# Performance work log

Measured on AMD Instinct MI355X. Metric: run time of the kernel, lower is better.

Reference implementation:

```python
import jax, jax.numpy as jnp
import numpy as np

B, K = 32768, 9  # batch, sudoku size


def setup_inputs() -> dict:
    key = jax.random.key(0)
    k1, = jax.random.split(key, 1)
    # binary possibility masks, as the module expects 0/1 sudoku tensors
    sudoku = (jax.random.uniform(k1, (B, K, K, K)) > 0.5).astype(jnp.float32)
    return {
        "sudoku": sudoku,
        "recursion_mask": jnp.zeros((B, K, K, K), jnp.float32),
        "recursion_index": jnp.ones((B, 1, 1, 1), jnp.float32),
        "conv_w": jnp.ones((1, K, 1, 1), jnp.float32),
        "conv_b": jnp.zeros((1,), jnp.float32),
    }


def reference(sudoku, recursion_mask, recursion_index, conv_w, conv_b):
    b = sudoku.shape[0]

    def conv1x1(x):  # channel-sum 1x1 conv: [b,K,K,K] -> [b,1,K,K]
        return jnp.sum(x * conv_w.reshape(1, K, 1, 1), axis=1, keepdims=True) + conv_b.reshape(1, 1, 1, 1)

    # number of candidates in each cell, minus 1, negated; empty cells pushed to -K
    nic = jax.nn.relu(conv1x1(sudoku) - 1.0)
    mask0 = jnp.clip(1.0 - jnp.abs(nic), 0.0, 1.0) * (-K)  # NNCompare(nic, 0) * -K
    nic = mask0 - nic  # [b,1,K,K]

    # MaxPool2d(K) + MaxUnpool2d(K): one-hot at the (first) argmax cell of the board
    idx = jnp.argmax(nic.reshape(b, K * K), axis=-1)
    current_cell_mask = jax.nn.one_hot(idx, K * K, dtype=sudoku.dtype).reshape(b, 1, K, K)

    # SudokuSelectOneVariant: per-cell MaxPool1d(K)+unpool over the number channel
    s = jnp.transpose(sudoku, (0, 3, 2, 1)).reshape(b, K * K, K)  # [b, cells, numbers]
    mval = jnp.max(s, axis=-1)
    midx = jnp.argmax(s, axis=-1)
    filt = jax.nn.one_hot(midx, K, dtype=sudoku.dtype) * mval[..., None]
    filt = jnp.transpose(filt.reshape(b, K, K, K), (0, 3, 2, 1))  # back to [b,K,K,K]
    one_variant = filt * current_cell_mask

    # mark all other candidates in the chosen cell, remove them from sudoku
    cell_mask = jnp.clip(conv1x1(one_variant), 0.0, 1.0)
    one_recursion_mask = sudoku * cell_mask * (1.0 - one_variant)  # NNAnd(.., NNNot(..))
    recursion_mask = jnp.maximum(recursion_mask, recursion_index * one_recursion_mask)
    recursion_mask = jnp.maximum(recursion_mask, (recursion_index - 1.0) * one_variant)
    sudoku_out = sudoku * (1.0 - one_recursion_mask)
    return sudoku_out, recursion_mask, recursion_index + 1.0
```

## Files before the change

kernel.cpp:

```cpp
#include <hip/hip_runtime.h>

typedef float v4f __attribute__((ext_vector_type(4)));

#define BDIM   256
#define KK     9
#define CELLS  81
#define BOARD  729
#define BPB    4
#define CHUNK  (BPB * BOARD)
#define LDSW   736

__global__ __launch_bounds__(BDIM) void sudoku_iter_kernel(
    const float* __restrict__ sudoku,
    const float* __restrict__ rmask,
    const float* __restrict__ rindex,
    const float* __restrict__ conv_w,
    const float* __restrict__ conv_b,
    float* __restrict__ out,
    int Btot)
{
    __shared__ float lds_s[BPB * LDSW];

    const int tid  = threadIdx.x;
    const int wave = tid >> 6;
    const int lane = tid & 63;
    const int blk  = blockIdx.x;
    const size_t base = (size_t)blk * CHUNK;

    const int fstart = wave * BOARD;
    const int g_lo   = (fstart + 3) >> 2;
    const int g_hi   = (fstart + BOARD) >> 2;
    const int h      = 4 * g_lo - fstart;
    const int t      = fstart + BOARD - 4 * g_hi;
    const int n4     = g_hi - g_lo;

    const v4f* gs4 = (const v4f*)(sudoku + base);
    const v4f* gr4 = (const v4f*)(rmask  + base);
    v4f s4[3], r4[3];
    bool act[3];
    #pragma unroll
    for (int i = 0; i < 3; ++i) {
        int k2 = lane + 64 * i;
        act[i] = (k2 < n4);
        if (act[i]) s4[i] = gs4[g_lo + k2];
    }
    const bool hasH = (lane < h);
    const bool hasT = (lane >= 8) && (lane < 8 + t);
    const int  eH   = lane;
    const int  eT   = BOARD - t + (lane - 8);
    float sh = 0.f, st = 0.f, rh = 0.f, rt = 0.f;
    if (hasH) sh = sudoku[base + fstart + eH];
    if (hasT) st = sudoku[base + fstart + eT];
    #pragma unroll
    for (int i = 0; i < 3; ++i) {
        if (act[i]) r4[i] = gr4[g_lo + lane + 64 * i];
    }
    if (hasH) rh = rmask[base + fstart + eH];
    if (hasT) rt = rmask[base + fstart + eT];
    float ri0 = (lane == 0) ? rindex[blk * BPB + wave] : 0.f;

    float wreg[KK];
    #pragma unroll
    for (int n = 0; n < KK; ++n) wreg[n] = conv_w[n];
    const float bias = conv_b[0];
    const float cmp  = fminf(fmaxf(bias, 0.f), 1.f);

    float* bs  = lds_s + wave * LDSW + (4 - h);
    v4f*   bs4 = (v4f*)(lds_s + wave * LDSW + 4);
    #pragma unroll
    for (int i = 0; i < 3; ++i) {
        if (act[i]) bs4[lane + 64 * i] = s4[i];
    }
    if (hasH) bs[eH] = sh;
    if (hasT) bs[eT] = st;

    float v0; int i0;
    {
        const int cell = lane;
        float cnt = bias;
        #pragma unroll
        for (int n = 0; n < KK; ++n) cnt += bs[n * CELLS + cell] * wreg[n];
        float nic = fmaxf(cnt - 1.f, 0.f);
        float m0  = fminf(fmaxf(1.f - nic, 0.f), 1.f) * (-(float)KK);
        v0 = m0 - nic; i0 = cell;
    }
    if (lane < CELLS - 64) {
        const int cell = lane + 64;
        float cnt = bias;
        #pragma unroll
        for (int n = 0; n < KK; ++n) cnt += bs[n * CELLS + cell] * wreg[n];
        float nic = fmaxf(cnt - 1.f, 0.f);
        float m0  = fminf(fmaxf(1.f - nic, 0.f), 1.f) * (-(float)KK);
        float v1 = m0 - nic;
        if (v1 > v0) { v0 = v1; i0 = cell; }
    }
    #pragma unroll
    for (int off = 32; off > 0; off >>= 1) {
        float ov = __shfl_xor(v0, off, 64);
        int   oi = __shfl_xor(i0, off, 64);
        if (ov > v0 || (ov == v0 && oi < i0)) { v0 = ov; i0 = oi; }
    }
    float m = 0.f, cms = 0.f; int es = 0, cellstar = 0;
    if (lane == 0) {
        cellstar = i0;
        m = bs[cellstar]; int nstar = 0;
        #pragma unroll
        for (int n = 1; n < KK; ++n) {
            float v = bs[n * CELLS + cellstar];
            if (v > m) { m = v; nstar = n; }
        }
        es  = nstar * CELLS + cellstar;
        cms = fminf(fmaxf(m * wreg[nstar] + bias, 0.f), 1.f);
    }
    m        = __shfl(m, 0, 64);
    cms      = __shfl(cms, 0, 64);
    es       = __shfl(es, 0, 64);
    cellstar = __shfl(cellstar, 0, 64);
    const float ri = __shfl(ri0, 0, 64);

    v4f* os4 = (v4f*)(out + base);
    v4f* or4 = (v4f*)(out + (size_t)Btot * BOARD + base);
    const int ebase = h + 4 * lane;
    const int cbase = ebase % CELLS;
    const int iadd[3] = {0, 13, 26};

    #pragma unroll
    for (int i = 0; i < 3; ++i) {
        if (act[i]) {
            float so[4], ro[4];
            const float* sp = (const float*)&s4[i];
            const float* rp = (const float*)&r4[i];
            #pragma unroll
            for (int j = 0; j < 4; ++j) {
                int e = ebase + 256 * i + j;
                int cell = cbase + iadd[i] + j;
                if (cell >= CELLS) cell -= CELLS;
                float s  = sp[j];
                float rm = rp[j];
                float ov  = (e == es) ? m : 0.f;
                float cm  = (cell == cellstar) ? cms : cmp;
                float orm = s * cm * (1.f - ov);
                float rmo = fmaxf(rm, ri * orm);
                rmo = fmaxf(rmo, (ri - 1.f) * ov);
                so[j] = s * (1.f - orm);
                ro[j] = rmo;
            }
            v4f sv; sv.x = so[0]; sv.y = so[1]; sv.z = so[2]; sv.w = so[3];
            v4f rv; rv.x = ro[0]; rv.y = ro[1]; rv.z = ro[2]; rv.w = ro[3];
            __builtin_nontemporal_store(sv, &os4[g_lo + lane + 64 * i]);
            __builtin_nontemporal_store(rv, &or4[g_lo + lane + 64 * i]);
        }
    }
    if (hasH | hasT) {
        int   e  = hasH ? eH : eT;
        float s  = hasH ? sh : st;
        float rm = hasH ? rh : rt;
        int cell = (e >= 648) ? (e - 648) : e;
        float ov  = (e == es) ? m : 0.f;
        float cm  = (cell == cellstar) ? cms : cmp;
        float orm = s * cm * (1.f - ov);
        float rmo = fmaxf(rm, ri * orm);
        rmo = fmaxf(rmo, (ri - 1.f) * ov);
        __builtin_nontemporal_store(s * (1.f - orm), out + base + fstart + e);
        __builtin_nontemporal_store(rmo, out + (size_t)Btot * BOARD + base + fstart + e);
    }

    if (lane == 0) {
        out[(size_t)Btot * BOARD * 2 + (size_t)blk * BPB + wave] = ri + 1.f;
    }
}

extern "C" void kernel_launch(void* const* d_in, const int* in_sizes, int n_in,
                              void* d_out, int out_size, void* d_ws, size_t ws_size,
                              hipStream_t stream) {
    const float* sudoku = (const float*)d_in[0];
    const float* rmask  = (const float*)d_in[1];
    const float* rindex = (const float*)d_in[2];
    const float* conv_w = (const float*)d_in[3];
    const float* conv_b = (const float*)d_in[4];
    float* out = (float*)d_out;

    const int Btot = in_sizes[2];
    const int nblocks = Btot / BPB;

    sudoku_iter_kernel<<<nblocks, BDIM, 0, stream>>>(
        sudoku, rmask, rindex, conv_w, conv_b, out, Btot);
}
```

Before: 336.4 us.

## Drop LDS staging; read cell columns directly from global and reload after argmax

Removes the shared-memory board buffer. Each wave now loads its 9 channel values per cell straight from global memory (strided scalar loads), computes the argmax, then each lane reads the chosen cell column itself instead of lane 0 broadcasting it. The vectorised sudoku/rmask loads now happen after the argmax and re-read the board, which is meant to hit in cache. This trades LDS traffic and shuffles for extra global (cache) loads and a serialised second read phase.

Result: no change. 330.1 us (-1.9%).

```diff
diff --git a/kernel.cpp b/kernel.cpp
--- a/kernel.cpp
+++ b/kernel.cpp
@@ -7,8 +7,6 @@
 #define CELLS  81
 #define BOARD  729
 #define BPB    4
-#define CHUNK  (BPB * BOARD)
-#define LDSW   736
 
 __global__ __launch_bounds__(BDIM) void sudoku_iter_kernel(
     const float* __restrict__ sudoku,
@@ -19,80 +17,44 @@
     float* __restrict__ out,
     int Btot)
 {
-    __shared__ float lds_s[BPB * LDSW];
+    const int tid   = threadIdx.x;
+    const int lane  = tid & 63;
+    const int board = blockIdx.x * BPB + (tid >> 6);
+    const unsigned fs = (unsigned)board * BOARD;
+    const float* bs = sudoku + fs;
 
-    const int tid  = threadIdx.x;
-    const int wave = tid >> 6;
-    const int lane = tid & 63;
-    const int blk  = blockIdx.x;
-    const size_t base = (size_t)blk * CHUNK;
-
-    const int fstart = wave * BOARD;
-    const int g_lo   = (fstart + 3) >> 2;
-    const int g_hi   = (fstart + BOARD) >> 2;
-    const int h      = 4 * g_lo - fstart;
-    const int t      = fstart + BOARD - 4 * g_hi;
-    const int n4     = g_hi - g_lo;
-
-    const v4f* gs4 = (const v4f*)(sudoku + base);
-    const v4f* gr4 = (const v4f*)(rmask  + base);
-    v4f s4[3], r4[3];
-    bool act[3];
+    float a[KK];
     #pragma unroll
-    for (int i = 0; i < 3; ++i) {
-        int k2 = lane + 64 * i;
-        act[i] = (k2 < n4);
-        if (act[i]) s4[i] = gs4[g_lo + k2];
-    }
-    const bool hasH = (lane < h);
-    const bool hasT = (lane >= 8) && (lane < 8 + t);
-    const int  eH   = lane;
-    const int  eT   = BOARD - t + (lane - 8);
-    float sh = 0.f, st = 0.f, rh = 0.f, rt = 0.f;
-    if (hasH) sh = sudoku[base + fstart + eH];
-    if (hasT) st = sudoku[base + fstart + eT];
+    for (int n = 0; n < KK; ++n) a[n] = bs[n * CELLS + lane];
+    const bool hi = (lane < CELLS - 64);
+    float b[KK];
     #pragma unroll
-    for (int i = 0; i < 3; ++i) {
-        if (act[i]) r4[i] = gr4[g_lo + lane + 64 * i];
-    }
-    if (hasH) rh = rmask[base + fstart + eH];
-    if (hasT) rt = rmask[base + fstart + eT];
-    float ri0 = (lane == 0) ? rindex[blk * BPB + wave] : 0.f;
+    for (int n = 0; n < KK; ++n) b[n] = hi ? bs[n * CELLS + 64 + lane] : 0.f;
 
     float wreg[KK];
     #pragma unroll
     for (int n = 0; n < KK; ++n) wreg[n] = conv_w[n];
     const float bias = conv_b[0];
     const float cmp  = fminf(fmaxf(bias, 0.f), 1.f);
-
-    float* bs  = lds_s + wave * LDSW + (4 - h);
-    v4f*   bs4 = (v4f*)(lds_s + wave * LDSW + 4);
-    #pragma unroll
-    for (int i = 0; i < 3; ++i) {
-        if (act[i]) bs4[lane + 64 * i] = s4[i];
-    }
-    if (hasH) bs[eH] = sh;
-    if (hasT) bs[eT] = st;
+    const float ri   = rindex[board];
 
     float v0; int i0;
     {
-        const int cell = lane;
         float cnt = bias;
         #pragma unroll
-        for (int n = 0; n < KK; ++n) cnt += bs[n * CELLS + cell] * wreg[n];
+        for (int n = 0; n < KK; ++n) cnt += a[n] * wreg[n];
         float nic = fmaxf(cnt - 1.f, 0.f);
         float m0  = fminf(fmaxf(1.f - nic, 0.f), 1.f) * (-(float)KK);
-        v0 = m0 - nic; i0 = cell;
+        v0 = m0 - nic; i0 = lane;
     }
-    if (lane < CELLS - 64) {
-        const int cell = lane + 64;
+    if (hi) {
         float cnt = bias;
         #pragma unroll
-        for (int n = 0; n < KK; ++n) cnt += bs[n * CELLS + cell] * wreg[n];
+        for (int n = 0; n < KK; ++n) cnt += b[n] * wreg[n];
         float nic = fmaxf(cnt - 1.f, 0.f);
         float m0  = fminf(fmaxf(1.f - nic, 0.f), 1.f) * (-(float)KK);
         float v1 = m0 - nic;
-        if (v1 > v0) { v0 = v1; i0 = cell; }
+        if (v1 > v0) { v0 = v1; i0 = lane + 64; }
     }
     #pragma unroll
     for (int off = 32; off > 0; off >>= 1) {
@@ -100,28 +62,49 @@
         int   oi = __shfl_xor(i0, off, 64);
         if (ov > v0 || (ov == v0 && oi < i0)) { v0 = ov; i0 = oi; }
     }
-    float m = 0.f, cms = 0.f; int es = 0, cellstar = 0;
-    if (lane == 0) {
-        cellstar = i0;
-        m = bs[cellstar]; int nstar = 0;
-        #pragma unroll
-        for (int n = 1; n < KK; ++n) {
-            float v = bs[n * CELLS + cellstar];
-            if (v > m) { m = v; nstar = n; }
-        }
-        es  = nstar * CELLS + cellstar;
-        cms = fminf(fmaxf(m * wreg[nstar] + bias, 0.f), 1.f);
+    const int cellstar = __builtin_amdgcn_readfirstlane(i0);
+
+    float m = bs[cellstar]; int nstar = 0;
+    #pragma unroll
+    for (int n = 1; n < KK; ++n) {
+        float v = bs[n * CELLS + cellstar];
+        if (v > m) { m = v; nstar = n; }
     }
-    m        = __shfl(m, 0, 64);
-    cms      = __shfl(cms, 0, 64);
-    es       = __shfl(es, 0, 64);
-    cellstar = __shfl(cellstar, 0, 64);
-    const float ri = __shfl(ri0, 0, 64);
+    const int   es  = nstar * CELLS + cellstar;
+    const float cms = fminf(fmaxf(m * wreg[nstar] + bias, 0.f), 1.f);
 
-    v4f* os4 = (v4f*)(out + base);
-    v4f* or4 = (v4f*)(out + (size_t)Btot * BOARD + base);
-    const int ebase = h + 4 * lane;
-    const int cbase = ebase % CELLS;
+    const unsigned G_lo = (fs + 3) >> 2;
+    const unsigned G_hi = (fs + BOARD) >> 2;
+    const int h  = (int)(4 * G_lo - fs);
+    const int t  = (int)(fs + BOARD - 4 * G_hi);
+    const int n4 = (int)(G_hi - G_lo);
+
+    const v4f* gs4 = (const v4f*)sudoku;
+    const v4f* gr4 = (const v4f*)rmask;
+    v4f* os4 = (v4f*)out;
+    v4f* or4 = (v4f*)(out + (size_t)Btot * BOARD);
+
+    v4f s4[3], r4[3];
+    bool act[3];
+    #pragma unroll
+    for (int i = 0; i < 3; ++i) {
+        int k = lane + 64 * i;
+        act[i] = (k < n4);
+        if (act[i]) s4[i] = gs4[G_lo + k];
+    }
+    #pragma unroll
+    for (int i = 0; i < 3; ++i) {
+        if (act[i]) r4[i] = gr4[G_lo + lane + 64 * i];
+    }
+    const bool hasH = (lane < h);
+    const bool hasT = (lane >= 8) && (lane < 8 + t);
+    const int  eH   = lane;
+    const int  eT   = BOARD - t + (lane - 8);
+    float shd = 0.f, std_ = 0.f, rhd = 0.f, rtd = 0.f;
+    if (hasH) { shd = sudoku[fs + eH]; rhd = rmask[fs + eH]; }
+    if (hasT) { std_ = sudoku[fs + eT]; rtd = rmask[fs + eT]; }
+
+    const int cbase = (h + 4 * lane) % CELLS;
     const int iadd[3] = {0, 13, 26};
 
     #pragma unroll
@@ -132,7 +115,7 @@
             const float* rp = (const float*)&r4[i];
             #pragma unroll
             for (int j = 0; j < 4; ++j) {
-                int e = ebase + 256 * i + j;
+                int e = h + 4 * (lane + 64 * i) + j;
                 int cell = cbase + iadd[i] + j;
                 if (cell >= CELLS) cell -= CELLS;
                 float s  = sp[j];
@@ -147,26 +130,27 @@
             }
             v4f sv; sv.x = so[0]; sv.y = so[1]; sv.z = so[2]; sv.w = so[3];
             v4f rv; rv.x = ro[0]; rv.y = ro[1]; rv.z = ro[2]; rv.w = ro[3];
-            __builtin_nontemporal_store(sv, &os4[g_lo + lane + 64 * i]);
-            __builtin_nontemporal_store(rv, &or4[g_lo + lane + 64 * i]);
+            unsigned g = G_lo + lane + 64 * i;
+            __builtin_nontemporal_store(sv, &os4[g]);
+            __builtin_nontemporal_store(rv, &or4[g]);
         }
     }
     if (hasH | hasT) {
         int   e  = hasH ? eH : eT;
-        float s  = hasH ? sh : st;
-        float rm = hasH ? rh : rt;
+        float s  = hasH ? shd : std_;
+        float rm = hasH ? rhd : rtd;
         int cell = (e >= 648) ? (e - 648) : e;
         float ov  = (e == es) ? m : 0.f;
         float cm  = (cell == cellstar) ? cms : cmp;
         float orm = s * cm * (1.f - ov);
         float rmo = fmaxf(rm, ri * orm);
         rmo = fmaxf(rmo, (ri - 1.f) * ov);
-        __builtin_nontemporal_store(s * (1.f - orm), out + base + fstart + e);
-        __builtin_nontemporal_store(rmo, out + (size_t)Btot * BOARD + base + fstart + e);
+        __builtin_nontemporal_store(s * (1.f - orm), out + fs + e);
+        __builtin_nontemporal_store(rmo, out + (size_t)Btot * BOARD + fs + e);
     }
 
     if (lane == 0) {
-        out[(size_t)Btot * BOARD * 2 + (size_t)blk * BPB + wave] = ri + 1.f;
+        out[(size_t)Btot * BOARD * 2 + board] = ri + 1.f;
     }
 }
 
```
